# Performance work log

Hardware: AMD Instinct MI355X
Metric: run time of the kernel (lower is better)

Reference implementation:

```python
import jax, jax.numpy as jnp
import numpy as np


def _bn(x, g, b):
    # per-feature batch norm over (batch, seq), training-style statistics
    mu = jnp.mean(x, axis=(0, 1), keepdims=True)
    var = jnp.var(x, axis=(0, 1), keepdims=True)
    return (x - mu) * jax.lax.rsqrt(var + 1e-5) * g + b


def _heads(x, H):
    B, S, D = x.shape
    return x.reshape(B, S, H, D // H).transpose(0, 2, 1, 3)  # [B,H,S,hd]


def _merge(x):
    B, H, S, hd = x.shape
    return x.transpose(0, 2, 1, 3).reshape(B, S, H * hd)


def _pos_encoding(S, D, dtype):
    p = jnp.arange(S, dtype=jnp.float32)[:, None]
    i = jnp.arange(D // 2, dtype=jnp.float32)[None, :]
    ang = p / jnp.power(10000.0, 2.0 * i / D)
    # interleave sin (even dims) and cos (odd dims)
    return jnp.stack([jnp.sin(ang), jnp.cos(ang)], axis=-1).reshape(S, D).astype(dtype)


def _forward(x, encod, embed, Wq, bq, Wk, bk, Wv, bv, g1, b1,
             Wq2, bq2, Wk2, bk2, Wv2, bv2, Wo2, bo2, g2, b2, Wf, bf,
             num_heads, N):
    D = embed.shape[1]
    emb = embed[x]                      # [B,S,D]
    S = emb.shape[1]
    # forward does embed + (embed + pos) == 2*embed + pos
    input_multi = 2.0 * emb + _pos_encoding(S, D, emb.dtype)
    scale1 = 1.0 / np.sqrt(D)           # original scales by sqrt(embed_dim)
    scale2 = 1.0 / np.sqrt(D // num_heads)
    for _ in range(N):
        q, k, v = jnp.split(input_multi, 3, axis=-1)   # each [B,S,D/3]
        Q = _heads(jax.nn.relu(q @ Wq + bq), num_heads)
        K = _heads(jax.nn.relu(k @ Wk + bk), num_heads)
        Vm = _heads(jax.nn.relu(v @ Wv + bv), num_heads)
        A = jax.nn.softmax(jnp.einsum('bhqd,bhkd->bhqk', Q, K) * scale1, axis=-1)
        sa = _merge(jnp.einsum('bhqk,bhkd->bhqd', A, Vm))
        t = _bn(input_multi + sa, g1, b1)
        # cross attention: q,k from encoder halves, v from decoder state
        eq, ek = jnp.split(encod, 2, axis=-1)          # each [B,S,D/2]
        Q2 = _heads(eq @ Wq2 + bq2, num_heads)
        K2 = _heads(ek @ Wk2 + bk2, num_heads)
        V2 = _heads(t @ Wv2 + bv2, num_heads)
        A2 = jax.nn.softmax(jnp.einsum('bhqd,bhkd->bhqk', Q2, K2) * scale2, axis=-1)
        m2 = _merge(jnp.einsum('bhqk,bhkd->bhqd', A2, V2)) @ Wo2 + bo2
        t = _bn(m2 + t, g2, b2)
        # add_norm_2 reused for the FFN residual, as in the source
        input_multi = _bn(t + (t @ Wf + bf), g2, b2)
    return input_multi


def setup_inputs() -> dict:
    B, S, D, H, V, N = 4, 1024, 768, 12, 32000, 2
    ks = jax.random.split(jax.random.key(0), 12)
    w = lambda k, shape: jax.random.normal(k, shape, jnp.float32) * 0.02
    zeros = lambda: jnp.zeros((D,), jnp.float32)
    ones = lambda: jnp.ones((D,), jnp.float32)
    return {
        'x': jax.random.randint(ks[0], (B, S), 0, V),
        'encod': jax.random.normal(ks[1], (B, S, D), jnp.float32),
        'embed': w(ks[2], (V, D)),
        'Wq': w(ks[3], (D // 3, D)), 'bq': zeros(),
        'Wk': w(ks[4], (D // 3, D)), 'bk': zeros(),
        'Wv': w(ks[5], (D // 3, D)), 'bv': zeros(),
        'g1': ones(), 'b1': zeros(),
        'Wq2': w(ks[6], (D // 2, D)), 'bq2': zeros(),
        'Wk2': w(ks[7], (D // 2, D)), 'bk2': zeros(),
        'Wv2': w(ks[8], (D, D)), 'bv2': zeros(),
        'Wo2': w(ks[9], (D, D)), 'bo2': zeros(),
        'g2': ones(), 'b2': zeros(),
        'Wf': w(ks[10], (D, D)), 'bf': zeros(),
        'num_heads': H, 'N': N,
    }


def reference(x, encod, embed, Wq, bq, Wk, bk, Wv, bv, g1, b1,
              Wq2, bq2, Wk2, bk2, Wv2, bv2, Wo2, bo2, g2, b2, Wf, bf,
              num_heads, N):
    return _forward(x, encod, embed, Wq, bq, Wk, bk, Wv, bv, g1, b1,
                    Wq2, bq2, Wk2, bk2, Wv2, bv2, Wo2, bo2, g2, b2, Wf, bf,
                    num_heads, N)
```

## Files before the change

kernel.cpp:

```cpp
#include <hip/hip_runtime.h>
#include <hip/hip_bf16.h>

#define B 4
#define S 1024
#define D 768
#define H 12
#define HD 64
#define MROWS (B * S)
#define NELEM (B * S * D)

typedef __attribute__((ext_vector_type(8))) short short8;
typedef __attribute__((ext_vector_type(4))) short s16x4;
typedef __attribute__((ext_vector_type(4))) float f32x4;

#define MFMA16(a, b, c) __builtin_amdgcn_mfma_f32_16x16x32_bf16(a, b, c, 0, 0, 0)

#define SWZ64(row, col)  ((col) ^ (((row) & 7) << 3))
#define SWZ32(row, col)  ((col) ^ ((((row) >> 1) & 3) << 3))
#define SWZ128(row, col) ((col) ^ (((row) & 15) << 3))

static __device__ __forceinline__ float bs2f(short s) {
    unsigned int u = ((unsigned int)(unsigned short)s) << 16;
    float f;
    __builtin_memcpy(&f, &u, 4);
    return f;
}
static __device__ __forceinline__ short f2bs(float f) {
    __hip_bfloat16 h = __float2bfloat16(f);
    return __builtin_bit_cast(short, h);
}
static __device__ __forceinline__ float loadin(const void* p, size_t i, int isb) {
    return isb ? bs2f(((const short*)p)[i]) : ((const float*)p)[i];
}

__global__ void detect_k(const void* p, int* flag) {
    const short* hb = (const short*)p;
    int t = threadIdx.x;
    int ins = 0;
    #pragma unroll
    for (int j = 0; j < 4; j++) {
        float v = bs2f(hb[(t * 4 + j) * 2]);
        if (!(v == v) || fabsf(v) > 1e3f || (v != 0.0f && fabsf(v) < 1e-20f)) ins++;
    }
    #pragma unroll
    for (int off = 32; off; off >>= 1) ins += __shfl_xor(ins, off);
    if (t == 0) *flag = (ins > 64) ? 0 : 1;
}

__global__ __launch_bounds__(256) void embed_pos_k(const int* __restrict__ x,
                                                   const void* __restrict__ embed,
                                                   float* __restrict__ outf,
                                                   short* __restrict__ outb,
                                                   const int* __restrict__ flg) {
    const int f = *flg;
    int bs = blockIdx.x;
    int tok = x[bs];
    int s = bs & (S - 1);
    for (int j = threadIdx.x; j < D; j += 256) {
        float e = loadin(embed, (size_t)tok * D + j, f);
        int i = j >> 1;
        float ang = (float)s * __expf(-9.210340371976184f * (2.0f * (float)i) / (float)D);
        float p = (j & 1) ? cosf(ang) : sinf(ang);
        float v = 2.0f * e + p;
        outf[bs * D + j] = v;
        outb[bs * D + j] = f2bs(v);
    }
}

struct WSegs {
    const void* src[8];
    short* dst[8];
    int K[8];
    const void* esrc;
    short* edst;
    float* statz;
};

__global__ __launch_bounds__(256) void prep_k(WSegs sg, const int* __restrict__ flg) {
    const int f = *flg;
    const int seg = blockIdx.z;
    const int t = threadIdx.x;
    if (seg == 8) {
        int tid = (blockIdx.y * 12 + blockIdx.x) * 256 + t;
        if (tid < 1536) sg.statz[tid] = 0.f;
        for (int i = tid; i < NELEM; i += 12 * 12 * 256)
            sg.edst[i] = f2bs(loadin(sg.esrc, i, f));
        return;
    }
    const int K = sg.K[seg];
    const int k0 = blockIdx.y * 64;
    if (k0 >= K) return;
    const void* src = sg.src[seg];
    short* dst = sg.dst[seg];
    __shared__ __align__(16) short Ts[64 * 72];
    int n0 = blockIdx.x * 64;
    int r = t >> 2, c4 = (t & 3) * 16;
    #pragma unroll
    for (int j = 0; j < 16; j++)
        Ts[r * 72 + c4 + j] = f2bs(loadin(src, (size_t)(k0 + r) * D + n0 + c4 + j, f));
    __syncthreads();
    int n = t >> 2, kc = (t & 3) * 16;
    short tmp[16];
    #pragma unroll
    for (int j = 0; j < 16; j++) tmp[j] = Ts[(kc + j) * 72 + n];
    short* dchunk = dst + (size_t)(n0 + n) * K + k0 + kc;
    *(short8*)&dchunk[0] = *(const short8*)&tmp[0];
    *(short8*)&dchunk[8] = *(const short8*)&tmp[8];
}

__global__ __launch_bounds__(256) void bnprep_k(float* __restrict__ sums,
                                                const void* __restrict__ g,
                                                const void* __restrict__ beta,
                                                float* __restrict__ ss,
                                                const int* __restrict__ flg) {
    const int fl = *flg;
    int f = blockIdx.x * 256 + threadIdx.x;
    if (f < D) {
        float s = sums[f], s2 = sums[D + f];
        float mean = s * (1.0f / (float)MROWS);
        float var = s2 * (1.0f / (float)MROWS) - mean * mean;
        float rstd = rsqrtf(var + 1e-5f);
        float sc = rstd * loadin(g, f, fl);
        ss[f] = sc;
        ss[D + f] = loadin(beta, f, fl) - mean * sc;
        sums[f] = 0.f;
        sums[D + f] = 0.f;
    }
}

__global__ __launch_bounds__(256) void store_norm_k(const float* __restrict__ a,
                                                    const float* __restrict__ ss,
                                                    void* __restrict__ out,
                                                    const int* __restrict__ flg) {
    const int f = *flg;
    int i = blockIdx.x * 256 + threadIdx.x;
    if (i < NELEM) {
        int ft = i % D;
        float y = a[i] * ss[ft] + ss[D + ft];
        if (f) ((short*)out)[i] = f2bs(y);
        else   ((float*)out)[i] = y;
    }
}

struct GJob {
    const void* A;
    const short* WT;
    const void* bias;
    void* out;
    const float* resid;
    const float* rss;
    const float* ass;
    float* sacc;
    int K;
    int aoff;
    int relu;
    int mode;
};
struct GJobs { GJob j[3]; };

__global__ __launch_bounds__(256) void mgemm_k(GJobs js, const int* __restrict__ flg) {
    const GJob J = js.j[blockIdx.z];
    const int f = *flg;
    __shared__ __align__(16) short sb[64 * 72];
    short* As = sb;
    short* Bs = sb + 2048;
    const int t = threadIdx.x;
    const int wave = t >> 6, lane = t & 63;
    const int quad = lane >> 4, l16 = lane & 15;
    int lin = blockIdx.y * gridDim.x + blockIdx.x;
    int per = (gridDim.x * gridDim.y) >> 3;
    int nl = (lin & 7) * per + (lin >> 3);
    const int n0 = (nl % gridDim.x) * 64;
    const int m0 = (nl / gridDim.x) * 64;
    const int wm = (wave >> 1) * 32;
    const int wn = (wave & 1) * 32;
    f32x4 acc[2][2];
    #pragma unroll
    for (int i = 0; i < 2; i++)
        #pragma unroll
        for (int j = 0; j < 2; j++) acc[i][j] = f32x4{0.f, 0.f, 0.f, 0.f};

    const int ar = t >> 2;
    const int ac = (t & 3) * 8;
    const int acs = SWZ32(ar, ac);
    const int K = J.K;
    for (int k0 = 0; k0 < K; k0 += 32) {
        if (J.ass) {
            int ft = J.aoff + k0 + ac;
            const float* Af = (const float*)J.A + (size_t)(m0 + ar) * 768 + ft;
            f32x4 v0 = *(const f32x4*)&Af[0];
            f32x4 v1 = *(const f32x4*)&Af[4];
            f32x4 sc0 = *(const f32x4*)&J.ass[ft];
            f32x4 sc1 = *(const f32x4*)&J.ass[ft + 4];
            f32x4 sh0 = *(const f32x4*)&J.ass[D + ft];
            f32x4 sh1 = *(const f32x4*)&J.ass[D + ft + 4];
            short8 pk;
            #pragma unroll
            for (int e = 0; e < 4; e++) {
                pk[e]     = f2bs(v0[e] * sc0[e] + sh0[e]);
                pk[4 + e] = f2bs(v1[e] * sc1[e] + sh1[e]);
            }
            *(short8*)&As[ar * 32 + acs] = pk;
        } else {
            *(short8*)&As[ar * 32 + acs] =
                *(const short8*)&((const short*)J.A)[(size_t)(m0 + ar) * 768 + k0 + ac];
        }
        *(short8*)&Bs[ar * 32 + SWZ32(ar, ac)] =
            *(const short8*)&J.WT[(size_t)(n0 + ar) * K + k0 + ac];
        __syncthreads();
        short8 af[2], bfr[2];
        #pragma unroll
        for (int i = 0; i < 2; i++) {
            int arow = wm + i * 16 + l16;
            af[i] = *(const short8*)&As[arow * 32 + SWZ32(arow, quad * 8)];
        }
        #pragma unroll
        for (int j = 0; j < 2; j++) {
            int brow = wn + j * 16 + l16;
            bfr[j] = *(const short8*)&Bs[brow * 32 + SWZ32(brow, quad * 8)];
        }
        #pragma unroll
        for (int i = 0; i < 2; i++)
            #pragma unroll
            for (int j = 0; j < 2; j++)
                acc[i][j] = MFMA16(af[i], bfr[j], acc[i][j]);
        __syncthreads();
    }
    if (J.mode == 3) {
        #pragma unroll
        for (int j = 0; j < 2; j++) {
            int coll = wn + j * 16 + l16;
            float bv = loadin(J.bias, n0 + coll, f);
            #pragma unroll
            for (int i = 0; i < 2; i++) {
                int rowl = wm + i * 16 + quad * 4;
                s16x4 pk;
                #pragma unroll
                for (int r = 0; r < 4; r++) {
                    float v = acc[i][j][r] + bv;
                    if (J.relu) v = fmaxf(v, 0.f);
                    pk[r] = f2bs(v);
                }
                *(s16x4*)&sb[coll * 72 + rowl] = pk;
            }
        }
        __syncthreads();
        int hd = t >> 2, c = (t & 3) * 16;
        int b = m0 >> 10, s0 = m0 & (S - 1), h = n0 >> 6;
        short* dst = (short*)J.out + (((size_t)(b * H + h) * HD + hd) * S + s0 + c);
        *(short8*)&dst[0] = *(const short8*)&sb[hd * 72 + c];
        *(short8*)&dst[8] = *(const short8*)&sb[hd * 72 + c + 8];
    } else {
        #pragma unroll
        for (int j = 0; j < 2; j++) {
            int col = n0 + wn + j * 16 + l16;
            float bv = loadin(J.bias, col, f);
            float rsc = 1.f, rsh = 0.f;
            if (J.rss) { rsc = J.rss[col]; rsh = J.rss[D + col]; }
            float s1 = 0.f, s2 = 0.f;
            #pragma unroll
            for (int i = 0; i < 2; i++) {
                int rowb = m0 + wm + i * 16 + quad * 4;
                #pragma unroll
                for (int r = 0; r < 4; r++) {
                    float v = acc[i][j][r] + bv;
                    if (J.relu) v = fmaxf(v, 0.f);
                    int row = rowb + r;
                    if (J.mode == 2) {
                        size_t idx = (size_t)row * D + col;
                        if (J.resid) {
                            float rv = J.resid[idx];
                            v += J.rss ? (rv * rsc + rsh) : rv;
                        }
                        ((float*)J.out)[idx] = v;
                        s1 += v;
                        s2 += v * v;
                    } else if (J.mode == 1) {
                        size_t idx = (((size_t)(row >> 10) * H + (col >> 6)) * S + (row & (S - 1))) * HD + (col & 63);
                        ((short*)J.out)[idx] = f2bs(v);
                    } else {
                        ((short*)J.out)[(size_t)row * D + col] = f2bs(v);
                    }
                }
            }
            if (J.mode == 2 && J.sacc) {
                s1 += __shfl_xor(s1, 16); s1 += __shfl_xor(s1, 32);
                s2 += __shfl_xor(s2, 16); s2 += __shfl_xor(s2, 32);
                if (quad == 0) {
                    atomicAdd(&J.sacc[col], s1);
                    atomicAdd(&J.sacc[D + col], s2);
                }
            }
        }
    }
}

__global__ __launch_bounds__(256) void mfma_attn_fo_k(const short* __restrict__ Q,
                                                      const short* __restrict__ Km,
                                                      const short* __restrict__ Vt,
                                                      void* __restrict__ out,
                                                      const float* __restrict__ resid,
                                                      const float* __restrict__ rss,
                                                      float* __restrict__ sacc,
                                                      float scale, int obf) {
    __shared__ __align__(16) short Ks[128 * 64];
    __shared__ __align__(16) short Vs[64 * 128];
    __shared__ __align__(16) short Ps[4][16 * 136];
    const int qt = blockIdx.y;
    const int bh = blockIdx.x;
    const int b = bh / H, h = bh % H;
    const int t = threadIdx.x;
    const int wave = t >> 6, lane = t & 63, quad = lane >> 4, l16 = lane & 15;
    const float sc2 = scale * 1.44269504089f;
    const short* Qh = Q + (size_t)bh * S * HD;
    const short* Kh = Km + (size_t)bh * S * HD;
    const short* Vh = Vt + (size_t)bh * S * HD;
    const int qrow = qt * 64 + wave * 16 + l16;
    short8 qf0 = *(const short8*)&Qh[(size_t)qrow * 64 + quad * 8];
    short8 qf1 = *(const short8*)&Qh[(size_t)qrow * 64 + 32 + quad * 8];
    f32x4 o[4];
    float m_i[4], l_i[4];
    #pragma unroll
    for (int nt = 0; nt < 4; nt++) o[nt] = f32x4{0.f, 0.f, 0.f, 0.f};
    #pragma unroll
    for (int r = 0; r < 4; r++) { m_i[r] = -1e30f; l_i[r] = 0.f; }
    const int krow = t >> 1, kc0 = (t & 1) * 32;
    const int vhd = t >> 2, vkc = (t & 3) * 32;

    for (int kt = 0; kt < S; kt += 128) {
        const short* ksrc = &Kh[(size_t)(kt + krow) * 64 + kc0];
        #pragma unroll
        for (int j = 0; j < 4; j++)
            *(short8*)&Ks[krow * 64 + SWZ64(krow, kc0 + j * 8)] = *(const short8*)&ksrc[j * 8];
        const short* vsrc = &Vh[(size_t)vhd * S + kt + vkc];
        #pragma unroll
        for (int j = 0; j < 4; j++)
            *(short8*)&Vs[vhd * 128 + SWZ128(vhd, vkc + j * 8)] = *(const short8*)&vsrc[j * 8];
        __syncthreads();
        f32x4 sf[8];
        #pragma unroll
        for (int nt = 0; nt < 8; nt++) {
            int kr = nt * 16 + l16;
            short8 kb0 = *(const short8*)&Ks[kr * 64 + SWZ64(kr, quad * 8)];
            short8 kb1 = *(const short8*)&Ks[kr * 64 + SWZ64(kr, 32 + quad * 8)];
            f32x4 c = f32x4{0.f, 0.f, 0.f, 0.f};
            c = MFMA16(qf0, kb0, c);
            c = MFMA16(qf1, kb1, c);
            sf[nt] = c;
        }
        #pragma unroll
        for (int r = 0; r < 4; r++) {
            float mx = sf[0][r];
            #pragma unroll
            for (int nt = 1; nt < 8; nt++) mx = fmaxf(mx, sf[nt][r]);
            mx = fmaxf(mx, __shfl_xor(mx, 1));
            mx = fmaxf(mx, __shfl_xor(mx, 2));
            mx = fmaxf(mx, __shfl_xor(mx, 4));
            mx = fmaxf(mx, __shfl_xor(mx, 8));
            float mnew = fmaxf(m_i[r], mx);
            float alpha = exp2f((m_i[r] - mnew) * sc2);
            m_i[r] = mnew;
            float rs = 0.f;
            #pragma unroll
            for (int nt = 0; nt < 8; nt++) {
                float p = exp2f((sf[nt][r] - mnew) * sc2);
                sf[nt][r] = p;
                rs += p;
            }
            rs += __shfl_xor(rs, 1);
            rs += __shfl_xor(rs, 2);
            rs += __shfl_xor(rs, 4);
            rs += __shfl_xor(rs, 8);
            l_i[r] = l_i[r] * alpha + rs;
            #pragma unroll
            for (int nt = 0; nt < 4; nt++) o[nt][r] *= alpha;
        }
        #pragma unroll
        for (int nt = 0; nt < 8; nt++)
            #pragma unroll
            for (int r = 0; r < 4; r++)
                Ps[wave][(quad * 4 + r) * 136 + nt * 16 + l16] = f2bs(sf[nt][r]);
        short8 pa[4];
        #pragma unroll
        for (int kc = 0; kc < 4; kc++)
            pa[kc] = *(const short8*)&Ps[wave][l16 * 136 + kc * 32 + quad * 8];
        #pragma unroll
        for (int nt = 0; nt < 4; nt++) {
            int vr = nt * 16 + l16;
            #pragma unroll
            for (int kc = 0; kc < 4; kc++) {
                short8 vb = *(const short8*)&Vs[vr * 128 + SWZ128(vr, kc * 32 + quad * 8)];
                o[nt] = MFMA16(pa[kc], vb, o[nt]);
            }
        }
        __syncthreads();
    }
    float inv[4];
    #pragma unroll
    for (int r = 0; r < 4; r++) inv[r] = 1.0f / l_i[r];
    #pragma unroll
    for (int nt = 0; nt < 4; nt++) {
        int col = h * HD + nt * 16 + l16;
        float rsc = 1.f, rsh = 0.f;
        if (rss) { rsc = rss[col]; rsh = rss[D + col]; }
        float s1 = 0.f, s2 = 0.f;
        #pragma unroll
        for (int r = 0; r < 4; r++) {
            int row = b * S + qt * 64 + wave * 16 + quad * 4 + r;
            size_t idx = (size_t)row * D + col;
            float v = o[nt][r] * inv[r];
            if (obf) {
                ((short*)out)[idx] = f2bs(v);
            } else {
                if (resid) {
                    float rv = resid[idx];
                    v += rss ? (rv * rsc + rsh) : rv;
                }
                ((float*)out)[idx] = v;
                s1 += v;
                s2 += v * v;
            }
        }
        if (sacc) {
            s1 += __shfl_xor(s1, 16); s1 += __shfl_xor(s1, 32);
            s2 += __shfl_xor(s2, 16); s2 += __shfl_xor(s2, 32);
            if (quad == 0) {
                atomicAdd(&sacc[col], s1);
                atomicAdd(&sacc[D + col], s2);
            }
        }
    }
}

extern "C" void kernel_launch(void* const* d_in, const int* in_sizes, int n_in,
                              void* d_out, int out_size, void* d_ws, size_t ws_size,
                              hipStream_t stream) {
    const int* x = (const int*)d_in[0];
    const short* encod = (const short*)d_in[1];
    const short* embed = (const short*)d_in[2];
    const short* Wq = (const short*)d_in[3];
    const short* bq = (const short*)d_in[4];
    const short* Wk = (const short*)d_in[5];
    const short* bk = (const short*)d_in[6];
    const short* Wv = (const short*)d_in[7];
    const short* bv = (const short*)d_in[8];
    const short* g1 = (const short*)d_in[9];
    const short* b1 = (const short*)d_in[10];
    const short* Wq2 = (const short*)d_in[11];
    const short* bq2 = (const short*)d_in[12];
    const short* Wk2 = (const short*)d_in[13];
    const short* bk2 = (const short*)d_in[14];
    const short* Wv2 = (const short*)d_in[15];
    const short* bv2 = (const short*)d_in[16];
    const short* Wo2 = (const short*)d_in[17];
    const short* bo2 = (const short*)d_in[18];
    const short* g2 = (const short*)d_in[19];
    const short* b2 = (const short*)d_in[20];
    const short* Wf = (const short*)d_in[21];
    const short* bf_ = (const short*)d_in[22];

    short* HBase = (short*)d_ws;
    #define HB(i) (HBase + (size_t)(i) * NELEM)
    float* IMf = (float*)HB(0);
    short* IMb = HB(2);
    short* Q2h = HB(3);
    short* K2h = HB(4);
    short* WTp = HB(5);
    short* WTq  = WTp;
    short* WTk  = WTp + 196608;
    short* WTv  = WTp + 393216;
    short* WTq2 = WTp + 589824;
    short* WTk2 = WTp + 884736;
    short* WTv2 = WTp + 1179648;
    short* WTo2 = WTp + 1769472;
    short* WTf  = WTp + 2359296;
    short* Qbh = HB(6);
    short* Kbh = HB(7);
    short* Vth = HB(9);
    float* T1f = (float*)HB(10);
    float* Ff  = (float*)HB(12);
    short* A2b = HB(15);
    float* T2f = (float*)HB(16);
    short* Eb  = Qbh;
    float* fstats = (float*)HB(18);
    float* ssA  = fstats;
    float* ssB  = fstats + 2 * D;
    float* ssC  = fstats + 4 * D;
    float* sums = fstats + 6 * D;
    int*   flg  = (int*)(fstats + 8 * D);

    const dim3 gGrid(12, 64);
    const dim3 aGrid(B * H, S / 64);
    const int EB = (NELEM + 255) / 256;
    const float scale1 = 0.03608439182435161f;
    const float scale2 = 0.125f;

    detect_k<<<1, 64, 0, stream>>>(encod, flg);
    embed_pos_k<<<MROWS, 256, 0, stream>>>(x, embed, IMf, IMb, flg);

    WSegs sg;
    sg.src[0] = Wq;  sg.dst[0] = WTq;  sg.K[0] = 256;
    sg.src[1] = Wk;  sg.dst[1] = WTk;  sg.K[1] = 256;
    sg.src[2] = Wv;  sg.dst[2] = WTv;  sg.K[2] = 256;
    sg.src[3] = Wq2; sg.dst[3] = WTq2; sg.K[3] = 384;
    sg.src[4] = Wk2; sg.dst[4] = WTk2; sg.K[4] = 384;
    sg.src[5] = Wv2; sg.dst[5] = WTv2; sg.K[5] = 768;
    sg.src[6] = Wo2; sg.dst[6] = WTo2; sg.K[6] = 768;
    sg.src[7] = Wf;  sg.dst[7] = WTf;  sg.K[7] = 768;
    sg.esrc = encod; sg.edst = Eb; sg.statz = sums;
    prep_k<<<dim3(12, 12, 9), 256, 0, stream>>>(sg, flg);

    {
        GJobs js;
        js.j[0] = GJob{Eb,       WTq2, bq2, Q2h, nullptr, nullptr, nullptr, nullptr, 384, 0, 0, 1};
        js.j[1] = GJob{Eb + 384, WTk2, bk2, K2h, nullptr, nullptr, nullptr, nullptr, 384, 0, 0, 1};
        js.j[2] = js.j[0];
        mgemm_k<<<dim3(12, 64, 2), 256, 0, stream>>>(js, flg);
    }

    for (int it = 0; it < 2; it++) {
        {
            GJobs js;
            if (it == 0) {
                js.j[0] = GJob{IMb,       WTq, bq, Qbh, nullptr, nullptr, nullptr, nullptr, 256, 0,   1, 1};
                js.j[1] = GJob{IMb + 256, WTk, bk, Kbh, nullptr, nullptr, nullptr, nullptr, 256, 0,   1, 1};
                js.j[2] = GJob{IMb + 512, WTv, bv, Vth, nullptr, nullptr, nullptr, nullptr, 256, 0,   1, 3};
            } else {
                js.j[0] = GJob{Ff, WTq, bq, Qbh, nullptr, nullptr, ssC, nullptr, 256, 0,   1, 1};
                js.j[1] = GJob{Ff, WTk, bk, Kbh, nullptr, nullptr, ssC, nullptr, 256, 256, 1, 1};
                js.j[2] = GJob{Ff, WTv, bv, Vth, nullptr, nullptr, ssC, nullptr, 256, 512, 1, 3};
            }
            mgemm_k<<<dim3(12, 64, 3), 256, 0, stream>>>(js, flg);
        }
        if (it == 0)
            mfma_attn_fo_k<<<aGrid, 256, 0, stream>>>(Qbh, Kbh, Vth, T1f, IMf, nullptr, sums, scale1, 0);
        else
            mfma_attn_fo_k<<<aGrid, 256, 0, stream>>>(Qbh, Kbh, Vth, T1f, Ff, ssC, sums, scale1, 0);
        bnprep_k<<<3, 256, 0, stream>>>(sums, g1, b1, ssA, flg);
        {
            GJobs js;
            js.j[0] = GJob{T1f, WTv2, bv2, Vth, nullptr, nullptr, ssA, nullptr, 768, 0, 0, 3};
            js.j[1] = js.j[0]; js.j[2] = js.j[0];
            mgemm_k<<<gGrid, 256, 0, stream>>>(js, flg);
        }
        mfma_attn_fo_k<<<aGrid, 256, 0, stream>>>(Q2h, K2h, Vth, A2b, nullptr, nullptr, nullptr, scale2, 1);
        {
            GJobs js;
            js.j[0] = GJob{A2b, WTo2, bo2, T2f, T1f, ssA, nullptr, sums, 768, 0, 0, 2};
            js.j[1] = js.j[0]; js.j[2] = js.j[0];
            mgemm_k<<<gGrid, 256, 0, stream>>>(js, flg);
        }
        bnprep_k<<<3, 256, 0, stream>>>(sums, g2, b2, ssB, flg);
        {
            GJobs js;
            js.j[0] = GJob{T2f, WTf, bf_, Ff, T2f, ssB, ssB, sums, 768, 0, 0, 2};
            js.j[1] = js.j[0]; js.j[2] = js.j[0];
            mgemm_k<<<gGrid, 256, 0, stream>>>(js, flg);
        }
        bnprep_k<<<3, 256, 0, stream>>>(sums, g2, b2, ssC, flg);
    }

    store_norm_k<<<EB, 256, 0, stream>>>(Ff, ssC, d_out, flg);
}
```

Measured before the change: 671.2 us.

## Fold batch-norm prep into consumers, prefetch K/V tiles, use MFMA row sums in attention

Removes the separate bnprep kernels by giving each BN stage its own sums buffer and recomputing scale and shift inside the consuming GEMM, attention and store kernels, with the GEMM caching them in shared memory. In the attention kernel, the next K/V tile is prefetched into registers while the current one is computed. The row sum is now an MFMA against a ones vector, and the running max is rescaled lazily, only when the max jumps by more than a threshold. This cuts launch count and shuffle/exp work, at the cost of redundant per-block BN math, extra LDS, and a bf16 row sum that may lose precision.

Result: faster. 618.9 us (-7.8%).

```diff
diff --git a/kernel.cpp b/kernel.cpp
--- a/kernel.cpp
+++ b/kernel.cpp
@@ -82,7 +82,7 @@
     const int t = threadIdx.x;
     if (seg == 8) {
         int tid = (blockIdx.y * 12 + blockIdx.x) * 256 + t;
-        if (tid < 1536) sg.statz[tid] = 0.f;
+        if (tid < 9216) sg.statz[tid] = 0.f;
         for (int i = tid; i < NELEM; i += 12 * 12 * 256)
             sg.edst[i] = f2bs(loadin(sg.esrc, i, f));
         return;
@@ -108,35 +108,20 @@
     *(short8*)&dchunk[8] = *(const short8*)&tmp[8];
 }
 
-__global__ __launch_bounds__(256) void bnprep_k(float* __restrict__ sums,
-                                                const void* __restrict__ g,
-                                                const void* __restrict__ beta,
-                                                float* __restrict__ ss,
-                                                const int* __restrict__ flg) {
-    const int fl = *flg;
-    int f = blockIdx.x * 256 + threadIdx.x;
-    if (f < D) {
-        float s = sums[f], s2 = sums[D + f];
-        float mean = s * (1.0f / (float)MROWS);
-        float var = s2 * (1.0f / (float)MROWS) - mean * mean;
-        float rstd = rsqrtf(var + 1e-5f);
-        float sc = rstd * loadin(g, f, fl);
-        ss[f] = sc;
-        ss[D + f] = loadin(beta, f, fl) - mean * sc;
-        sums[f] = 0.f;
-        sums[D + f] = 0.f;
-    }
-}
-
 __global__ __launch_bounds__(256) void store_norm_k(const float* __restrict__ a,
-                                                    const float* __restrict__ ss,
+                                                    const float* __restrict__ sums,
+                                                    const void* __restrict__ g,
+                                                    const void* __restrict__ beta,
                                                     void* __restrict__ out,
                                                     const int* __restrict__ flg) {
     const int f = *flg;
     int i = blockIdx.x * 256 + threadIdx.x;
     if (i < NELEM) {
         int ft = i % D;
-        float y = a[i] * ss[ft] + ss[D + ft];
+        float mean = sums[ft] * (1.0f / (float)MROWS);
+        float var = sums[D + ft] * (1.0f / (float)MROWS) - mean * mean;
+        float sc = rsqrtf(var + 1e-5f) * loadin(g, ft, f);
+        float y = (a[i] - mean) * sc + loadin(beta, ft, f);
         if (f) ((short*)out)[i] = f2bs(y);
         else   ((float*)out)[i] = y;
     }
@@ -148,13 +133,16 @@
     const void* bias;
     void* out;
     const float* resid;
-    const float* rss;
-    const float* ass;
+    const float* bnsums;
+    const void* bng;
+    const void* bnb;
     float* sacc;
     int K;
     int aoff;
     int relu;
     int mode;
+    int anorm;
+    int rnorm;
 };
 struct GJobs { GJob j[3]; };
 
@@ -162,11 +150,23 @@
     const GJob J = js.j[blockIdx.z];
     const int f = *flg;
     __shared__ __align__(16) short sb[64 * 72];
+    __shared__ float ssb0[768];
+    __shared__ float ssb1[768];
     short* As = sb;
     short* Bs = sb + 2048;
     const int t = threadIdx.x;
     const int wave = t >> 6, lane = t & 63;
     const int quad = lane >> 4, l16 = lane & 15;
+    if (J.anorm) {
+        for (int i = t; i < D; i += 256) {
+            float mean = J.bnsums[i] * (1.0f / (float)MROWS);
+            float var = J.bnsums[D + i] * (1.0f / (float)MROWS) - mean * mean;
+            float sc = rsqrtf(var + 1e-5f) * loadin(J.bng, i, f);
+            ssb0[i] = sc;
+            ssb1[i] = loadin(J.bnb, i, f) - mean * sc;
+        }
+        __syncthreads();
+    }
     int lin = blockIdx.y * gridDim.x + blockIdx.x;
     int per = (gridDim.x * gridDim.y) >> 3;
     int nl = (lin & 7) * per + (lin >> 3);
@@ -185,15 +185,15 @@
     const int acs = SWZ32(ar, ac);
     const int K = J.K;
     for (int k0 = 0; k0 < K; k0 += 32) {
-        if (J.ass) {
+        if (J.anorm) {
             int ft = J.aoff + k0 + ac;
             const float* Af = (const float*)J.A + (size_t)(m0 + ar) * 768 + ft;
             f32x4 v0 = *(const f32x4*)&Af[0];
             f32x4 v1 = *(const f32x4*)&Af[4];
-            f32x4 sc0 = *(const f32x4*)&J.ass[ft];
-            f32x4 sc1 = *(const f32x4*)&J.ass[ft + 4];
-            f32x4 sh0 = *(const f32x4*)&J.ass[D + ft];
-            f32x4 sh1 = *(const f32x4*)&J.ass[D + ft + 4];
+            f32x4 sc0 = *(const f32x4*)&ssb0[ft];
+            f32x4 sc1 = *(const f32x4*)&ssb0[ft + 4];
+            f32x4 sh0 = *(const f32x4*)&ssb1[ft];
+            f32x4 sh1 = *(const f32x4*)&ssb1[ft + 4];
             short8 pk;
             #pragma unroll
             for (int e = 0; e < 4; e++) {
@@ -256,7 +256,12 @@
             int col = n0 + wn + j * 16 + l16;
             float bv = loadin(J.bias, col, f);
             float rsc = 1.f, rsh = 0.f;
-            if (J.rss) { rsc = J.rss[col]; rsh = J.rss[D + col]; }
+            if (J.rnorm) {
+                float mean = J.bnsums[col] * (1.0f / (float)MROWS);
+                float var = J.bnsums[D + col] * (1.0f / (float)MROWS) - mean * mean;
+                rsc = rsqrtf(var + 1e-5f) * loadin(J.bng, col, f);
+                rsh = loadin(J.bnb, col, f) - mean * rsc;
+            }
             float s1 = 0.f, s2 = 0.f;
             #pragma unroll
             for (int i = 0; i < 2; i++) {
@@ -270,7 +275,7 @@
                         size_t idx = (size_t)row * D + col;
                         if (J.resid) {
                             float rv = J.resid[idx];
-                            v += J.rss ? (rv * rsc + rsh) : rv;
+                            v += J.rnorm ? (rv * rsc + rsh) : rv;
                         }
                         ((float*)J.out)[idx] = v;
                         s1 += v;
@@ -300,12 +305,16 @@
                                                       const short* __restrict__ Vt,
                                                       void* __restrict__ out,
                                                       const float* __restrict__ resid,
-                                                      const float* __restrict__ rss,
+                                                      const float* __restrict__ rsums,
+                                                      const void* __restrict__ rg,
+                                                      const void* __restrict__ rb,
                                                       float* __restrict__ sacc,
-                                                      float scale, int obf) {
+                                                      float scale, int obf,
+                                                      const int* __restrict__ flg) {
     __shared__ __align__(16) short Ks[128 * 64];
     __shared__ __align__(16) short Vs[64 * 128];
     __shared__ __align__(16) short Ps[4][16 * 136];
+    const int fl = *flg;
     const int qt = blockIdx.y;
     const int bh = blockIdx.x;
     const int b = bh / H, h = bh % H;
@@ -318,25 +327,43 @@
     const int qrow = qt * 64 + wave * 16 + l16;
     short8 qf0 = *(const short8*)&Qh[(size_t)qrow * 64 + quad * 8];
     short8 qf1 = *(const short8*)&Qh[(size_t)qrow * 64 + 32 + quad * 8];
+    short8 ones;
+    #pragma unroll
+    for (int j = 0; j < 8; j++) ones[j] = (short)0x3F80;
     f32x4 o[4];
-    float m_i[4], l_i[4];
+    f32x4 ls = f32x4{0.f, 0.f, 0.f, 0.f};
+    float m_i[4];
     #pragma unroll
     for (int nt = 0; nt < 4; nt++) o[nt] = f32x4{0.f, 0.f, 0.f, 0.f};
     #pragma unroll
-    for (int r = 0; r < 4; r++) { m_i[r] = -1e30f; l_i[r] = 0.f; }
+    for (int r = 0; r < 4; r++) m_i[r] = -1e30f;
     const int krow = t >> 1, kc0 = (t & 1) * 32;
     const int vhd = t >> 2, vkc = (t & 3) * 32;
+    const short* kbase = &Kh[(size_t)krow * 64 + kc0];
+    const short* vbase = &Vh[(size_t)vhd * S + vkc];
+
+    short8 kreg[4], vreg[4];
+    #pragma unroll
+    for (int j = 0; j < 4; j++) kreg[j] = *(const short8*)&kbase[j * 8];
+    #pragma unroll
+    for (int j = 0; j < 4; j++) vreg[j] = *(const short8*)&vbase[j * 8];
+    #pragma unroll
+    for (int j = 0; j < 4; j++)
+        *(short8*)&Ks[krow * 64 + SWZ64(krow, kc0 + j * 8)] = kreg[j];
+    #pragma unroll
+    for (int j = 0; j < 4; j++)
+        *(short8*)&Vs[vhd * 128 + SWZ128(vhd, vkc + j * 8)] = vreg[j];
+    __syncthreads();
 
     for (int kt = 0; kt < S; kt += 128) {
-        const short* ksrc = &Kh[(size_t)(kt + krow) * 64 + kc0];
-        #pragma unroll
-        for (int j = 0; j < 4; j++)
-            *(short8*)&Ks[krow * 64 + SWZ64(krow, kc0 + j * 8)] = *(const short8*)&ksrc[j * 8];
-        const short* vsrc = &Vh[(size_t)vhd * S + kt + vkc];
-        #pragma unroll
-        for (int j = 0; j < 4; j++)
-            *(short8*)&Vs[vhd * 128 + SWZ128(vhd, vkc + j * 8)] = *(const short8*)&vsrc[j * 8];
-        __syncthreads();
+        if (kt + 128 < S) {
+            #pragma unroll
+            for (int j = 0; j < 4; j++)
+                kreg[j] = *(const short8*)&kbase[(size_t)(kt + 128) * 64 + j * 8];
+            #pragma unroll
+            for (int j = 0; j < 4; j++)
+                vreg[j] = *(const short8*)&vbase[kt + 128 + j * 8];
+        }
         f32x4 sf[8];
         #pragma unroll
         for (int nt = 0; nt < 8; nt++) {
@@ -348,38 +375,38 @@
             c = MFMA16(qf1, kb1, c);
             sf[nt] = c;
         }
+        float mx[4];
         #pragma unroll
         for (int r = 0; r < 4; r++) {
-            float mx = sf[0][r];
-            #pragma unroll
-            for (int nt = 1; nt < 8; nt++) mx = fmaxf(mx, sf[nt][r]);
-            mx = fmaxf(mx, __shfl_xor(mx, 1));
-            mx = fmaxf(mx, __shfl_xor(mx, 2));
-            mx = fmaxf(mx, __shfl_xor(mx, 4));
-            mx = fmaxf(mx, __shfl_xor(mx, 8));
-            float mnew = fmaxf(m_i[r], mx);
-            float alpha = exp2f((m_i[r] - mnew) * sc2);
-            m_i[r] = mnew;
-            float rs = 0.f;
-            #pragma unroll
-            for (int nt = 0; nt < 8; nt++) {
-                float p = exp2f((sf[nt][r] - mnew) * sc2);
-                sf[nt][r] = p;
-                rs += p;
-            }
-            rs += __shfl_xor(rs, 1);
-            rs += __shfl_xor(rs, 2);
-            rs += __shfl_xor(rs, 4);
-            rs += __shfl_xor(rs, 8);
-            l_i[r] = l_i[r] * alpha + rs;
-            #pragma unroll
-            for (int nt = 0; nt < 4; nt++) o[nt][r] *= alpha;
+            float m = sf[0][r];
+            #pragma unroll
+            for (int nt = 1; nt < 8; nt++) m = fmaxf(m, sf[nt][r]);
+            m = fmaxf(m, __shfl_xor(m, 1));
+            m = fmaxf(m, __shfl_xor(m, 2));
+            m = fmaxf(m, __shfl_xor(m, 4));
+            m = fmaxf(m, __shfl_xor(m, 8));
+            mx[r] = m;
+        }
+        bool need = false;
+        #pragma unroll
+        for (int r = 0; r < 4; r++) need |= ((mx[r] - m_i[r]) * sc2 > 8.0f);
+        if (__any(need)) {
+            #pragma unroll
+            for (int r = 0; r < 4; r++) {
+                float mnew = fmaxf(m_i[r], mx[r]);
+                float alpha = exp2f((m_i[r] - mnew) * sc2);
+                m_i[r] = mnew;
+                ls[r] *= alpha;
+                #pragma unroll
+                for (int nt = 0; nt < 4; nt++) o[nt][r] *= alpha;
+            }
         }
         #pragma unroll
         for (int nt = 0; nt < 8; nt++)
             #pragma unroll
             for (int r = 0; r < 4; r++)
-                Ps[wave][(quad * 4 + r) * 136 + nt * 16 + l16] = f2bs(sf[nt][r]);
+                Ps[wave][(quad * 4 + r) * 136 + nt * 16 + l16] =
+                    f2bs(exp2f((sf[nt][r] - m_i[r]) * sc2));
         short8 pa[4];
         #pragma unroll
         for (int kc = 0; kc < 4; kc++)
@@ -393,16 +420,32 @@
                 o[nt] = MFMA16(pa[kc], vb, o[nt]);
             }
         }
+        #pragma unroll
+        for (int kc = 0; kc < 4; kc++) ls = MFMA16(pa[kc], ones, ls);
         __syncthreads();
+        if (kt + 128 < S) {
+            #pragma unroll
+            for (int j = 0; j < 4; j++)
+                *(short8*)&Ks[krow * 64 + SWZ64(krow, kc0 + j * 8)] = kreg[j];
+            #pragma unroll
+            for (int j = 0; j < 4; j++)
+                *(short8*)&Vs[vhd * 128 + SWZ128(vhd, vkc + j * 8)] = vreg[j];
+        }
+        __syncthreads();
     }
     float inv[4];
     #pragma unroll
-    for (int r = 0; r < 4; r++) inv[r] = 1.0f / l_i[r];
+    for (int r = 0; r < 4; r++) inv[r] = 1.0f / ls[r];
     #pragma unroll
     for (int nt = 0; nt < 4; nt++) {
         int col = h * HD + nt * 16 + l16;
         float rsc = 1.f, rsh = 0.f;
-        if (rss) { rsc = rss[col]; rsh = rss[D + col]; }
+        if (rsums) {
+            float mean = rsums[col] * (1.0f / (float)MROWS);
+            float var = rsums[D + col] * (1.0f / (float)MROWS) - mean * mean;
+            rsc = rsqrtf(var + 1e-5f) * loadin(rg, col, fl);
+            rsh = loadin(rb, col, fl) - mean * rsc;
+        }
         float s1 = 0.f, s2 = 0.f;
         #pragma unroll
         for (int r = 0; r < 4; r++) {
@@ -414,7 +457,7 @@
             } else {
                 if (resid) {
                     float rv = resid[idx];
-                    v += rss ? (rv * rsc + rsh) : rv;
+                    v += rsums ? (rv * rsc + rsh) : rv;
                 }
                 ((float*)out)[idx] = v;
                 s1 += v;
@@ -482,12 +525,9 @@
     short* A2b = HB(15);
     float* T2f = (float*)HB(16);
     short* Eb  = Qbh;
-    float* fstats = (float*)HB(18);
-    float* ssA  = fstats;
-    float* ssB  = fstats + 2 * D;
-    float* ssC  = fstats + 4 * D;
-    float* sums = fstats + 6 * D;
-    int*   flg  = (int*)(fstats + 8 * D);
+    float* SU = (float*)HB(18);
+    #define SUMS(it, bn) (SU + (size_t)((it) * 3 + (bn)) * 2 * D)
+    int*   flg  = (int*)(SU + 12 * D);
 
     const dim3 gGrid(12, 64);
     const dim3 aGrid(B * H, S / 64);
@@ -507,13 +547,13 @@
     sg.src[5] = Wv2; sg.dst[5] = WTv2; sg.K[5] = 768;
     sg.src[6] = Wo2; sg.dst[6] = WTo2; sg.K[6] = 768;
     sg.src[7] = Wf;  sg.dst[7] = WTf;  sg.K[7] = 768;
-    sg.esrc = encod; sg.edst = Eb; sg.statz = sums;
+    sg.esrc = encod; sg.edst = Eb; sg.statz = SU;
     prep_k<<<dim3(12, 12, 9), 256, 0, stream>>>(sg, flg);
 
     {
         GJobs js;
-        js.j[0] = GJob{Eb,       WTq2, bq2, Q2h, nullptr, nullptr, nullptr, nullptr, 384, 0, 0, 1};
-        js.j[1] = GJob{Eb + 384, WTk2, bk2, K2h, nullptr, nullptr, nullptr, nullptr, 384, 0, 0, 1};
+        js.j[0] = GJob{Eb,       WTq2, bq2, Q2h, nullptr, nullptr, nullptr, nullptr, nullptr, 384, 0, 0, 1, 0, 0};
+        js.j[1] = GJob{Eb + 384, WTk2, bk2, K2h, nullptr, nullptr, nullptr, nullptr, nullptr, 384, 0, 0, 1, 0, 0};
         js.j[2] = js.j[0];
         mgemm_k<<<dim3(12, 64, 2), 256, 0, stream>>>(js, flg);
     }
@@ -522,43 +562,43 @@
         {
             GJobs js;
             if (it == 0) {
-                js.j[0] = GJob{IMb,       WTq, bq, Qbh, nullptr, nullptr, nullptr, nullptr, 256, 0,   1, 1};
-                js.j[1] = GJob{IMb + 256, WTk, bk, Kbh, nullptr, nullptr, nullptr, nullptr, 256, 0,   1, 1};
-                js.j[2] = GJob{IMb + 512, WTv, bv, Vth, nullptr, nullptr, nullptr, nullptr, 256, 0,   1, 3};
+                js.j[0] = GJob{IMb,       WTq, bq, Qbh, nullptr, nullptr, nullptr, nullptr, nullptr, 256, 0,   1, 1, 0, 0};
+                js.j[1] = GJob{IMb + 256, WTk, bk, Kbh, nullptr, nullptr, nullptr, nullptr, nullptr, 256, 0,   1, 1, 0, 0};
+                js.j[2] = GJob{IMb + 512, WTv, bv, Vth, nullptr, nullptr, nullptr, nullptr, nullptr, 256, 0,   1, 3, 0, 0};
             } else {
-                js.j[0] = GJob{Ff, WTq, bq, Qbh, nullptr, nullptr, ssC, nullptr, 256, 0,   1, 1};
-                js.j[1] = GJob{Ff, WTk, bk, Kbh, nullptr, nullptr, ssC, nullptr, 256, 256, 1, 1};
-                js.j[2] = GJob{Ff, WTv, bv, Vth, nullptr, nullptr, ssC, nullptr, 256, 512, 1, 3};
+                js.j[0] = GJob{Ff, WTq, bq, Qbh, nullptr, SUMS(0, 2), g2, b2, nullptr, 256, 0,   1, 1, 1, 0};
+                js.j[1] = GJob{Ff, WTk, bk, Kbh, nullptr, SUMS(0, 2), g2, b2, nullptr, 256, 256, 1, 1, 1, 0};
+                js.j[2] = GJob{Ff, WTv, bv, Vth, nullptr, SUMS(0, 2), g2, b2, nullptr, 256, 512, 1, 3, 1, 0};
             }
             mgemm_k<<<dim3(12, 64, 3), 256, 0, stream>>>(js, flg);
         }
         if (it == 0)
-            mfma_attn_fo_k<<<aGrid, 256, 0, stream>>>(Qbh, Kbh, Vth, T1f, IMf, nullptr, sums, scale1, 0);
+            mfma_attn_fo_k<<<aGrid, 256, 0, stream>>>(Qbh, Kbh, Vth, T1f, IMf,
+                    nullptr, nullptr, nullptr, SUMS(0, 0), scale1, 0, flg);
         else
-            mfma_attn_fo_k<<<aGrid, 256, 0, stream>>>(Qbh, Kbh, Vth, T1f, Ff, ssC, sums, scale1, 0);
-        bnprep_k<<<3, 256, 0, stream>>>(sums, g1, b1, ssA, flg);
+            mfma_attn_fo_k<<<aGrid, 256, 0, stream>>>(Qbh, Kbh, Vth, T1f, Ff,
+                    SUMS(0, 2), g2, b2, SUMS(1, 0), scale1, 0, flg);
         {
             GJobs js;
-            js.j[0] = GJob{T1f, WTv2, bv2, Vth, nullptr, nullptr, ssA, nullptr, 768, 0, 0, 3};
+            js.j[0] = GJob{T1f, WTv2, bv2, Vth, nullptr, SUMS(it, 0), g1, b1, nullptr, 768, 0, 0, 3, 1, 0};
             js.j[1] = js.j[0]; js.j[2] = js.j[0];
             mgemm_k<<<gGrid, 256, 0, stream>>>(js, flg);
         }
-        mfma_attn_fo_k<<<aGrid, 256, 0, stream>>>(Q2h, K2h, Vth, A2b, nullptr, nullptr, nullptr, scale2, 1);
+        mfma_attn_fo_k<<<aGrid, 256, 0, stream>>>(Q2h, K2h, Vth, A2b, nullptr,
+                nullptr, nullptr, nullptr, nullptr, scale2, 1, flg);
         {
             GJobs js;
-            js.j[0] = GJob{A2b, WTo2, bo2, T2f, T1f, ssA, nullptr, sums, 768, 0, 0, 2};
+            js.j[0] = GJob{A2b, WTo2, bo2, T2f, T1f, SUMS(it, 0), g1, b1, SUMS(it, 1), 768, 0, 0, 2, 0, 1};
             js.j[1] = js.j[0]; js.j[2] = js.j[0];
             mgemm_k<<<gGrid, 256, 0, stream>>>(js, flg);
         }
-        bnprep_k<<<3, 256, 0, stream>>>(sums, g2, b2, ssB, flg);
         {
             GJobs js;
-            js.j[0] = GJob{T2f, WTf, bf_, Ff, T2f, ssB, ssB, sums, 768, 0, 0, 2};
+            js.j[0] = GJob{T2f, WTf, bf_, Ff, T2f, SUMS(it, 1), g2, b2, SUMS(it, 2), 768, 0, 0, 2, 1, 1};
             js.j[1] = js.j[0]; js.j[2] = js.j[0];
             mgemm_k<<<gGrid, 256, 0, stream>>>(js, flg);
         }
-        bnprep_k<<<3, 256, 0, stream>>>(sums, g2, b2, ssC, flg);
-    }
-
-    store_norm_k<<<EB, 256, 0, stream>>>(Ff, ssC, d_out, flg);
-}
+    }
+
+    store_norm_k<<<EB, 256, 0, stream>>>(Ff, SUMS(1, 2), g2, b2, d_out, flg);
+}
```
